# Kernel optimization log

Measured on AMD Instinct MI355X. Metric: run time of the kernel, lower is better.

Reference implementation:

```python
import jax, jax.numpy as jnp
import numpy as np

N, E, G, H, V, L = 100000, 1000000, 1000, 128, 64, 4
NEG_SLOPE = 0.2

def lrelu(x):
    return jnp.where(x >= 0, x, NEG_SLOPE * x)

def setup_inputs() -> dict:
    key = jax.random.key(0)
    ks = jax.random.split(key, 24)
    s = 0.05
    inp = {
        'nfeats': jax.random.randint(ks[0], (N, 9), 0, V, dtype=jnp.int32),
        'efeats': jax.random.randint(ks[1], (E, 3), 0, 4, dtype=jnp.int32),
        'src': jax.random.randint(ks[2], (E,), 0, N, dtype=jnp.int32),
        'dst': jax.random.randint(ks[3], (E,), 0, N, dtype=jnp.int32),
        'graph_ids': jnp.sort(jax.random.randint(ks[4], (N,), 0, G, dtype=jnp.int32)),
        'atom_emb': jax.random.normal(ks[5], (9, V, H), jnp.float32) * s,
        'Wq': jax.random.normal(ks[6], (L, H, H), jnp.float32) * s,
        'bq': jnp.zeros((L, H), jnp.float32),
        'Wk': jax.random.normal(ks[7], (L, H, H), jnp.float32) * s,
        'bk': jnp.zeros((L, H), jnp.float32),
        'Wr': jax.random.normal(ks[8], (L, H, H), jnp.float32) * s,
        'br': jnp.zeros((L, H), jnp.float32),
        'W1': jax.random.normal(ks[9], (H, H // 2), jnp.float32) * s,
        'b1': jnp.zeros((H // 2,), jnp.float32),
        'g1': jnp.ones((H // 2,), jnp.float32),
        'beta1': jnp.zeros((H // 2,), jnp.float32),
        'W2': jax.random.normal(ks[10], (H // 2, H // 4), jnp.float32) * s,
        'b2': jnp.zeros((H // 4,), jnp.float32),
        'g2': jnp.ones((H // 4,), jnp.float32),
        'beta2': jnp.zeros((H // 4,), jnp.float32),
        'W3': jax.random.normal(ks[11], (H // 4, 1), jnp.float32) * s,
        'b3': jnp.zeros((1,), jnp.float32),
    }
    return inp

def batchnorm(x, g, b):
    mu = jnp.mean(x, axis=0)
    var = jnp.var(x, axis=0)
    return (x - mu) * jax.lax.rsqrt(var + 1e-5) * g + b

def reference(nfeats, efeats, src, dst, graph_ids, atom_emb, Wq, bq, Wk, bk, Wr, br,
              W1, b1, g1, beta1, W2, b2, g2, beta2, W3, b3):
    # AtomEncoder: sum of per-feature embeddings -> [N, H]
    h = jnp.sum(atom_emb[jnp.arange(9)[None, :], nfeats], axis=1)
    for l in range(L):
        q = h @ Wq[l] + bq[l]            # dst-side transform [N,H]
        k = h @ Wk[l] + bk[l]            # src-side transform [N,H]
        m = lrelu(q[dst] + k[src])       # per-edge message [E,H]
        agg = jax.ops.segment_sum(m, dst, num_segments=N)  # [N,H]
        h = lrelu(agg @ Wr[l] + br[l])   # norm='none' -> identity, then activation
    hg = jax.ops.segment_sum(h, graph_ids, num_segments=G)  # sum pooling [G,H]
    x = lrelu(batchnorm(hg @ W1 + b1, g1, beta1))
    x = lrelu(batchnorm(x @ W2 + b2, g2, beta2))
    return x @ W3 + b3
```

## Files before the change

kernel.cpp:

```cpp
#include <hip/hip_runtime.h>

#define NN 100000
#define NP 100096
#define NE 1000000
#define NG 1000
#define H 128
#define NLAYER 4
#define NEG 0.2f
#define SCAN_BLOCKS 98

using short8 = __attribute__((ext_vector_type(8))) short;
using fx4 = __attribute__((ext_vector_type(4))) float;

__device__ __forceinline__ float lrelu(float x) { return x >= 0.f ? x : NEG * x; }

__device__ __forceinline__ unsigned short f2bf(float f) {
    union { float f; unsigned int u; } v;
    v.f = f;
    return (unsigned short)((v.u + 0x7fffu + ((v.u >> 16) & 1u)) >> 16);
}
__device__ __forceinline__ float bf2f(unsigned short h) {
    union { unsigned int u; float f; } v;
    v.u = ((unsigned int)h) << 16;
    return v.f;
}
__device__ __forceinline__ float bflo(unsigned int u) {
    union { unsigned int x; float f; } v;
    v.x = u << 16;
    return v.f;
}
__device__ __forceinline__ float bfhi(unsigned int u) {
    union { unsigned int x; float f; } v;
    v.x = u & 0xffff0000u;
    return v.f;
}

__global__ __launch_bounds__(256) void k_atom(const int* __restrict__ nfeats,
                                              const float* __restrict__ emb,
                                              unsigned short* __restrict__ h) {
    int node = blockIdx.x * 4 + (threadIdx.x >> 6);
    if (node >= NN) return;
    int lane = threadIdx.x & 63;
    int c = lane * 2;
    float ax = 0.f, ay = 0.f;
#pragma unroll
    for (int f = 0; f < 9; ++f) {
        int idx = nfeats[node * 9 + f];
        float2 e = *(const float2*)(emb + (size_t)((f << 6) + idx) * H + c);
        ax += e.x;
        ay += e.y;
    }
    unsigned int packed = (unsigned int)f2bf(ax) | ((unsigned int)f2bf(ay) << 16);
    *(unsigned int*)(h + (size_t)node * H + c) = packed;
}

__global__ __launch_bounds__(256) void k_wt(const float* __restrict__ Wq,
                                            const float* __restrict__ Wk,
                                            const float* __restrict__ Wr,
                                            unsigned short* __restrict__ WT) {
    int mat = blockIdx.x;
    int l = mat / 3;
    int kind = mat - l * 3;
    const float* src = (kind == 0 ? Wq : kind == 1 ? Wk : Wr) + (size_t)l * H * H;
    unsigned short* dst = WT + (size_t)mat * H * H;
    for (int idx = threadIdx.x; idx < H * H; idx += 256) {
        int kk = idx >> 7, n = idx & 127;
        dst[n * H + kk] = f2bf(src[idx]);
    }
}

__global__ __launch_bounds__(256) void k_hist(const int* __restrict__ dst, int* __restrict__ deg) {
    int i = blockIdx.x * blockDim.x + threadIdx.x;
    if (i < NE) atomicAdd(&deg[dst[i]], 1);
}

__global__ __launch_bounds__(1024) void k_scan1(const int* __restrict__ deg,
                                                int* __restrict__ rowp,
                                                int* __restrict__ bsum) {
    __shared__ int tmp[1024];
    int t = threadIdx.x;
    int i = blockIdx.x * 1024 + t;
    int v = (i < NN) ? deg[i] : 0;
    tmp[t] = v;
    __syncthreads();
    for (int off = 1; off < 1024; off <<= 1) {
        int u = (t >= off) ? tmp[t - off] : 0;
        __syncthreads();
        tmp[t] += u;
        __syncthreads();
    }
    if (i < NN) rowp[i] = tmp[t] - v;
    if (t == 1023) bsum[blockIdx.x] = tmp[1023];
}

__global__ __launch_bounds__(128) void k_scan2(int* __restrict__ bsum) {
    __shared__ int tmp[128];
    int t = threadIdx.x;
    int v = (t < SCAN_BLOCKS) ? bsum[t] : 0;
    tmp[t] = v;
    __syncthreads();
    for (int off = 1; off < 128; off <<= 1) {
        int u = (t >= off) ? tmp[t - off] : 0;
        __syncthreads();
        tmp[t] += u;
        __syncthreads();
    }
    if (t < SCAN_BLOCKS) bsum[t] = tmp[t] - v;
}

__global__ __launch_bounds__(256) void k_scan3(const int* __restrict__ bsum,
                                               int* __restrict__ rowp,
                                               int* __restrict__ cursor) {
    int i = blockIdx.x * blockDim.x + threadIdx.x;
    if (i < NN) {
        int v = rowp[i] + bsum[i >> 10];
        rowp[i] = v;
        cursor[i] = v;
    }
    if (i == 0) rowp[NN] = NE;
}

__global__ __launch_bounds__(256) void k_scatter(const int* __restrict__ src,
                                                 const int* __restrict__ dst,
                                                 int* __restrict__ cursor,
                                                 int* __restrict__ csr_src) {
    int i = blockIdx.x * blockDim.x + threadIdx.x;
    if (i < NE) {
        int pos = atomicAdd(&cursor[dst[i]], 1);
        csr_src[pos] = src[i];
    }
}

__global__ __launch_bounds__(256) void k_gbound(const int* __restrict__ gid,
                                                int* __restrict__ gstart) {
    int g = blockIdx.x * blockDim.x + threadIdx.x;
    if (g > NG) return;
    if (g == NG) { gstart[NG] = NN; return; }
    int lo = 0, hi = NN;
    while (lo < hi) {
        int mid = (lo + hi) >> 1;
        if (gid[mid] < g) lo = mid + 1; else hi = mid;
    }
    gstart[g] = lo;
}

__global__ __launch_bounds__(256) void k_qk_mfma(const unsigned short* __restrict__ h,
                                                 const unsigned short* __restrict__ WTq,
                                                 const float* __restrict__ bq,
                                                 const unsigned short* __restrict__ WTk,
                                                 const float* __restrict__ bk,
                                                 unsigned short* __restrict__ q,
                                                 unsigned short* __restrict__ k) {
    int lane = threadIdx.x & 63;
    int wave = threadIdx.x >> 6;
    int row0 = blockIdx.x * 128 + wave * 32;
    int lrow = lane & 15;
    int lk = (lane >> 4) << 3;

    short8 a[2][4];
#pragma unroll
    for (int rt = 0; rt < 2; ++rt)
#pragma unroll
        for (int ks = 0; ks < 4; ++ks)
            a[rt][ks] = *(const short8*)(h + (size_t)(row0 + rt * 16 + lrow) * H + ks * 32 + lk);

    fx4 aq[2][8], ak[2][8];
#pragma unroll
    for (int ct = 0; ct < 8; ++ct) {
        float vq = bq[ct * 16 + lrow];
        float vk = bk[ct * 16 + lrow];
#pragma unroll
        for (int rt = 0; rt < 2; ++rt) {
            aq[rt][ct] = fx4{vq, vq, vq, vq};
            ak[rt][ct] = fx4{vk, vk, vk, vk};
        }
    }

#pragma unroll
    for (int ks = 0; ks < 4; ++ks)
#pragma unroll
        for (int ct = 0; ct < 8; ++ct) {
            short8 wq = *(const short8*)(WTq + (ct * 16 + lrow) * H + ks * 32 + lk);
            short8 wk = *(const short8*)(WTk + (ct * 16 + lrow) * H + ks * 32 + lk);
#pragma unroll
            for (int rt = 0; rt < 2; ++rt) {
                aq[rt][ct] = __builtin_amdgcn_mfma_f32_16x16x32_bf16(a[rt][ks], wq, aq[rt][ct], 0, 0, 0);
                ak[rt][ct] = __builtin_amdgcn_mfma_f32_16x16x32_bf16(a[rt][ks], wk, ak[rt][ct], 0, 0, 0);
            }
        }

#pragma unroll
    for (int rt = 0; rt < 2; ++rt)
#pragma unroll
        for (int ct = 0; ct < 8; ++ct)
#pragma unroll
            for (int rg = 0; rg < 4; ++rg) {
                int r = row0 + rt * 16 + ((lane >> 4) << 2) + rg;
                if (r < NN) {
                    q[(size_t)r * H + ct * 16 + lrow] = f2bf(aq[rt][ct][rg]);
                    k[(size_t)r * H + ct * 16 + lrow] = f2bf(ak[rt][ct][rg]);
                }
            }
}

__global__ __launch_bounds__(256) void k_r_mfma(const unsigned short* __restrict__ agg,
                                                const unsigned short* __restrict__ WTr,
                                                const float* __restrict__ br,
                                                unsigned short* __restrict__ hout) {
    int lane = threadIdx.x & 63;
    int wave = threadIdx.x >> 6;
    int row0 = blockIdx.x * 128 + wave * 32;
    int lrow = lane & 15;
    int lk = (lane >> 4) << 3;

    short8 a[2][4];
#pragma unroll
    for (int rt = 0; rt < 2; ++rt)
#pragma unroll
        for (int ks = 0; ks < 4; ++ks)
            a[rt][ks] = *(const short8*)(agg + (size_t)(row0 + rt * 16 + lrow) * H + ks * 32 + lk);

    fx4 acc[2][8];
#pragma unroll
    for (int ct = 0; ct < 8; ++ct) {
        float v = br[ct * 16 + lrow];
#pragma unroll
        for (int rt = 0; rt < 2; ++rt) acc[rt][ct] = fx4{v, v, v, v};
    }

#pragma unroll
    for (int ks = 0; ks < 4; ++ks)
#pragma unroll
        for (int ct = 0; ct < 8; ++ct) {
            short8 w = *(const short8*)(WTr + (ct * 16 + lrow) * H + ks * 32 + lk);
#pragma unroll
            for (int rt = 0; rt < 2; ++rt)
                acc[rt][ct] = __builtin_amdgcn_mfma_f32_16x16x32_bf16(a[rt][ks], w, acc[rt][ct], 0, 0, 0);
        }

#pragma unroll
    for (int rt = 0; rt < 2; ++rt)
#pragma unroll
        for (int ct = 0; ct < 8; ++ct)
#pragma unroll
            for (int rg = 0; rg < 4; ++rg) {
                int r = row0 + rt * 16 + ((lane >> 4) << 2) + rg;
                if (r < NN)
                    hout[(size_t)r * H + ct * 16 + lrow] = f2bf(lrelu(acc[rt][ct][rg]));
            }
}

__global__ __launch_bounds__(256) void k_rqk_mfma(const unsigned short* __restrict__ agg,
                                                  const unsigned short* __restrict__ WTr,
                                                  const float* __restrict__ br,
                                                  const unsigned short* __restrict__ WTq,
                                                  const float* __restrict__ bq,
                                                  const unsigned short* __restrict__ WTk,
                                                  const float* __restrict__ bk,
                                                  unsigned short* __restrict__ q,
                                                  unsigned short* __restrict__ k) {
    __shared__ unsigned short hls[4][32][136];
    int lane = threadIdx.x & 63;
    int wave = threadIdx.x >> 6;
    int row0 = blockIdx.x * 128 + wave * 32;
    int lrow = lane & 15;
    int lk = (lane >> 4) << 3;

    short8 a[2][4];
#pragma unroll
    for (int rt = 0; rt < 2; ++rt)
#pragma unroll
        for (int ks = 0; ks < 4; ++ks)
            a[rt][ks] = *(const short8*)(agg + (size_t)(row0 + rt * 16 + lrow) * H + ks * 32 + lk);

    fx4 acc[2][8];
#pragma unroll
    for (int ct = 0; ct < 8; ++ct) {
        float v = br[ct * 16 + lrow];
#pragma unroll
        for (int rt = 0; rt < 2; ++rt) acc[rt][ct] = fx4{v, v, v, v};
    }

#pragma unroll
    for (int ks = 0; ks < 4; ++ks)
#pragma unroll
        for (int ct = 0; ct < 8; ++ct) {
            short8 w = *(const short8*)(WTr + (ct * 16 + lrow) * H + ks * 32 + lk);
#pragma unroll
            for (int rt = 0; rt < 2; ++rt)
                acc[rt][ct] = __builtin_amdgcn_mfma_f32_16x16x32_bf16(a[rt][ks], w, acc[rt][ct], 0, 0, 0);
        }

#pragma unroll
    for (int rt = 0; rt < 2; ++rt)
#pragma unroll
        for (int ct = 0; ct < 8; ++ct)
#pragma unroll
            for (int rg = 0; rg < 4; ++rg) {
                int lr = rt * 16 + ((lane >> 4) << 2) + rg;
                hls[wave][lr][ct * 16 + lrow] = f2bf(lrelu(acc[rt][ct][rg]));
            }

    short8 a2[2][4];
#pragma unroll
    for (int rt = 0; rt < 2; ++rt)
#pragma unroll
        for (int ks = 0; ks < 4; ++ks)
            a2[rt][ks] = *(const short8*)&hls[wave][rt * 16 + lrow][ks * 32 + lk];

    fx4 aq[2][8], ak[2][8];
#pragma unroll
    for (int ct = 0; ct < 8; ++ct) {
        float vq = bq[ct * 16 + lrow];
        float vk = bk[ct * 16 + lrow];
#pragma unroll
        for (int rt = 0; rt < 2; ++rt) {
            aq[rt][ct] = fx4{vq, vq, vq, vq};
            ak[rt][ct] = fx4{vk, vk, vk, vk};
        }
    }

#pragma unroll
    for (int ks = 0; ks < 4; ++ks)
#pragma unroll
        for (int ct = 0; ct < 8; ++ct) {
            short8 wq = *(const short8*)(WTq + (ct * 16 + lrow) * H + ks * 32 + lk);
            short8 wk = *(const short8*)(WTk + (ct * 16 + lrow) * H + ks * 32 + lk);
#pragma unroll
            for (int rt = 0; rt < 2; ++rt) {
                aq[rt][ct] = __builtin_amdgcn_mfma_f32_16x16x32_bf16(a2[rt][ks], wq, aq[rt][ct], 0, 0, 0);
                ak[rt][ct] = __builtin_amdgcn_mfma_f32_16x16x32_bf16(a2[rt][ks], wk, ak[rt][ct], 0, 0, 0);
            }
        }

#pragma unroll
    for (int rt = 0; rt < 2; ++rt)
#pragma unroll
        for (int ct = 0; ct < 8; ++ct)
#pragma unroll
            for (int rg = 0; rg < 4; ++rg) {
                int r = row0 + rt * 16 + ((lane >> 4) << 2) + rg;
                if (r < NN) {
                    q[(size_t)r * H + ct * 16 + lrow] = f2bf(aq[rt][ct][rg]);
                    k[(size_t)r * H + ct * 16 + lrow] = f2bf(ak[rt][ct][rg]);
                }
            }
}

__global__ __launch_bounds__(256) void k_agg(const unsigned short* __restrict__ q,
                                             const unsigned short* __restrict__ kk,
                                             const int* __restrict__ rowp,
                                             const int* __restrict__ csr_src,
                                             unsigned short* __restrict__ agg) {
    int node = blockIdx.x * 4 + (threadIdx.x >> 6);
    if (node >= NN) return;
    int lane = threadIdx.x & 63;
    int qt = lane >> 4;
    int ql = lane & 15;
    int start = rowp[node];
    int end = rowp[node + 1];

    uint4 qp = *(const uint4*)(q + (size_t)node * H + ql * 8);
    float qv0 = bflo(qp.x), qv1 = bfhi(qp.x), qv2 = bflo(qp.y), qv3 = bfhi(qp.y);
    float qv4 = bflo(qp.z), qv5 = bfhi(qp.z), qv6 = bflo(qp.w), qv7 = bfhi(qp.w);
    float a0 = 0.f, a1 = 0.f, a2 = 0.f, a3 = 0.f, a4 = 0.f, a5 = 0.f, a6 = 0.f, a7 = 0.f;

    for (int base = start; base < end; base += 64) {
        int cnt = end - base;
        if (cnt > 64) cnt = 64;
        int sid = (lane < cnt) ? csr_src[base + lane] : 0;
        int cnt4 = (cnt + 3) & ~3;
        for (int j = 0; j < cnt4; j += 4) {
            int jj = j + qt;
            int s = __shfl(sid, jj);
            uint4 kp = *(const uint4*)(kk + (size_t)s * H + ql * 8);
            if (jj < cnt) {
                a0 += lrelu(qv0 + bflo(kp.x));
                a1 += lrelu(qv1 + bfhi(kp.x));
                a2 += lrelu(qv2 + bflo(kp.y));
                a3 += lrelu(qv3 + bfhi(kp.y));
                a4 += lrelu(qv4 + bflo(kp.z));
                a5 += lrelu(qv5 + bfhi(kp.z));
                a6 += lrelu(qv6 + bflo(kp.w));
                a7 += lrelu(qv7 + bfhi(kp.w));
            }
        }
    }
    a0 += __shfl_xor(a0, 16); a0 += __shfl_xor(a0, 32);
    a1 += __shfl_xor(a1, 16); a1 += __shfl_xor(a1, 32);
    a2 += __shfl_xor(a2, 16); a2 += __shfl_xor(a2, 32);
    a3 += __shfl_xor(a3, 16); a3 += __shfl_xor(a3, 32);
    a4 += __shfl_xor(a4, 16); a4 += __shfl_xor(a4, 32);
    a5 += __shfl_xor(a5, 16); a5 += __shfl_xor(a5, 32);
    a6 += __shfl_xor(a6, 16); a6 += __shfl_xor(a6, 32);
    a7 += __shfl_xor(a7, 16); a7 += __shfl_xor(a7, 32);
    if (qt == 0) {
        uint4 o;
        o.x = (unsigned int)f2bf(a0) | ((unsigned int)f2bf(a1) << 16);
        o.y = (unsigned int)f2bf(a2) | ((unsigned int)f2bf(a3) << 16);
        o.z = (unsigned int)f2bf(a4) | ((unsigned int)f2bf(a5) << 16);
        o.w = (unsigned int)f2bf(a6) | ((unsigned int)f2bf(a7) << 16);
        *(uint4*)(agg + (size_t)node * H + ql * 8) = o;
    }
}

__global__ __launch_bounds__(256) void k_pool_seg(const unsigned short* __restrict__ h,
                                                  const int* __restrict__ gstart,
                                                  float* __restrict__ hg) {
    int g = blockIdx.x * 4 + (threadIdx.x >> 6);
    if (g >= NG) return;
    int lane = threadIdx.x & 63;
    int s = gstart[g], e = gstart[g + 1];
    float ax = 0.f, ay = 0.f;
    for (int n = s; n < e; ++n) {
        unsigned int hp = *(const unsigned int*)(h + (size_t)n * H + lane * 2);
        ax += bflo(hp);
        ay += bfhi(hp);
    }
    float2 o;
    o.x = ax;
    o.y = ay;
    *(float2*)(hg + (size_t)g * H + lane * 2) = o;
}

__global__ __launch_bounds__(256) void k_mlp1(const float* __restrict__ hg,
                                              const float* __restrict__ W1,
                                              const float* __restrict__ b1,
                                              float* __restrict__ x1) {
    __shared__ float W1s[128 * 64];
    __shared__ float hgs[4 * 128];
    int t = threadIdx.x;
    int g0 = blockIdx.x * 4;
#pragma unroll
    for (int i = 0; i < 32; ++i) W1s[t + i * 256] = W1[t + i * 256];
    for (int i = t; i < 4 * 128; i += 256) hgs[i] = hg[(size_t)g0 * H + i];
    __syncthreads();
    int g = t >> 6, c = t & 63;
    float acc = b1[c];
    const float* row = hgs + g * 128;
    for (int j = 0; j < 128; ++j) acc += row[j] * W1s[j * 64 + c];
    x1[(g0 + g) * 64 + c] = acc;
}

template <int C>
__global__ __launch_bounds__(1024) void k_bnstats(const float* __restrict__ x,
                                                  float* __restrict__ stats) {
    __shared__ float red[1024];
    __shared__ float mus[C];
    int t = threadIdx.x;
    int c = t & (C - 1), rc = t / C;
    const int R = 1024 / C;
    float s = 0.f;
    for (int g = rc; g < NG; g += R) s += x[g * C + c];
    red[t] = s;
    __syncthreads();
    if (t < C) {
        float S = 0.f;
        for (int i = 0; i < R; ++i) S += red[i * C + t];
        float mu = S / NG;
        mus[t] = mu;
        stats[t] = mu;
    }
    __syncthreads();
    float mu = mus[c];
    float s2 = 0.f;
    for (int g = rc; g < NG; g += R) {
        float d = x[g * C + c] - mu;
        s2 += d * d;
    }
    red[t] = s2;
    __syncthreads();
    if (t < C) {
        float Q = 0.f;
        for (int i = 0; i < R; ++i) Q += red[i * C + t];
        stats[C + t] = rsqrtf(Q / NG + 1e-5f);
    }
}

__global__ __launch_bounds__(256) void k_mlp2f(const float* __restrict__ x1,
                                               const float* __restrict__ st,
                                               const float* __restrict__ g1,
                                               const float* __restrict__ be1,
                                               const float* __restrict__ W2,
                                               const float* __restrict__ b2,
                                               float* __restrict__ x2) {
    __shared__ float W2s[64 * 32];
    __shared__ float x1s[8 * 64];
    int t = threadIdx.x;
    int g0 = blockIdx.x * 8;
#pragma unroll
    for (int i = 0; i < 8; ++i) W2s[t + i * 256] = W2[t + i * 256];
#pragma unroll
    for (int i = 0; i < 2; ++i) {
        int idx = t + i * 256;
        int c = idx & 63;
        float v = x1[(size_t)g0 * 64 + idx];
        v = (v - st[c]) * st[64 + c] * g1[c] + be1[c];
        x1s[idx] = lrelu(v);
    }
    __syncthreads();
    int g = t >> 5, c = t & 31;
    float acc = b2[c];
    const float* row = x1s + g * 64;
    for (int j = 0; j < 64; ++j) acc += row[j] * W2s[j * 32 + c];
    x2[(g0 + g) * 32 + c] = acc;
}

__global__ __launch_bounds__(256) void k_mlp3f(const float* __restrict__ x2,
                                               const float* __restrict__ st,
                                               const float* __restrict__ g2,
                                               const float* __restrict__ be2,
                                               const float* __restrict__ W3,
                                               const float* __restrict__ b3,
                                               float* __restrict__ out) {
    int g = blockIdx.x * blockDim.x + threadIdx.x;
    if (g >= NG) return;
    float acc = b3[0];
    for (int j = 0; j < 32; ++j) {
        float v = (x2[g * 32 + j] - st[j]) * st[32 + j] * g2[j] + be2[j];
        acc += lrelu(v) * W3[j];
    }
    out[g] = acc;
}

extern "C" void kernel_launch(void* const* d_in, const int* in_sizes, int n_in,
                              void* d_out, int out_size, void* d_ws, size_t ws_size,
                              hipStream_t stream) {
    const int* nfeats = (const int*)d_in[0];
    const int* src = (const int*)d_in[2];
    const int* dst = (const int*)d_in[3];
    const int* gid = (const int*)d_in[4];
    const float* emb = (const float*)d_in[5];
    const float* Wq = (const float*)d_in[6];
    const float* bq = (const float*)d_in[7];
    const float* Wk = (const float*)d_in[8];
    const float* bk = (const float*)d_in[9];
    const float* Wr = (const float*)d_in[10];
    const float* br = (const float*)d_in[11];
    const float* W1 = (const float*)d_in[12];
    const float* b1 = (const float*)d_in[13];
    const float* g1 = (const float*)d_in[14];
    const float* be1 = (const float*)d_in[15];
    const float* W2 = (const float*)d_in[16];
    const float* b2 = (const float*)d_in[17];
    const float* g2 = (const float*)d_in[18];
    const float* be2 = (const float*)d_in[19];
    const float* W3 = (const float*)d_in[20];
    const float* b3 = (const float*)d_in[21];
    float* out = (float*)d_out;

    size_t nh = (size_t)NP * H;
    unsigned short* P0 = (unsigned short*)d_ws;
    unsigned short* P1 = P0 + nh;
    unsigned short* P2 = P1 + nh;
    unsigned short* WT = P2 + nh;
    float* hg = (float*)(WT + 12 * H * H);
    float* x1 = hg + (size_t)NG * H;
    float* x2 = x1 + (size_t)NG * 64;
    float* st = x2 + (size_t)NG * 32;
    int* cursor = (int*)(st + 2 * 64);
    int* rowp = cursor + NN;
    int* bsum = rowp + NN + 1;
    int* csr_src = bsum + 128;
    int* gstart = csr_src + NE;

    hipMemsetAsync(cursor, 0, NN * sizeof(int), stream);
    k_hist<<<(NE + 255) / 256, 256, 0, stream>>>(dst, cursor);
    k_scan1<<<SCAN_BLOCKS, 1024, 0, stream>>>(cursor, rowp, bsum);
    k_scan2<<<1, 128, 0, stream>>>(bsum);
    k_scan3<<<(NN + 255) / 256, 256, 0, stream>>>(bsum, rowp, cursor);
    k_scatter<<<(NE + 255) / 256, 256, 0, stream>>>(src, dst, cursor, csr_src);
    k_gbound<<<(NG + 256) / 256, 256, 0, stream>>>(gid, gstart);

    k_wt<<<12, 256, 0, stream>>>(Wq, Wk, Wr, WT);
    k_atom<<<NN / 4, 256, 0, stream>>>(nfeats, emb, P0);

    const int NB = NP / 128;
    k_qk_mfma<<<NB, 256, 0, stream>>>(P0, WT + 0 * H * H, bq, WT + 1 * H * H, bk, P1, P2);
    for (int l = 0; l < NLAYER; ++l) {
        k_agg<<<(NN + 3) / 4, 256, 0, stream>>>(P1, P2, rowp, csr_src, P0);
        if (l < NLAYER - 1) {
            k_rqk_mfma<<<NB, 256, 0, stream>>>(P0, WT + (size_t)(l * 3 + 2) * H * H, br + l * H,
                                               WT + (size_t)((l + 1) * 3 + 0) * H * H, bq + (l + 1) * H,
                                               WT + (size_t)((l + 1) * 3 + 1) * H * H, bk + (l + 1) * H,
                                               P1, P2);
        } else {
            k_r_mfma<<<NB, 256, 0, stream>>>(P0, WT + (size_t)(l * 3 + 2) * H * H, br + l * H, P1);
        }
    }

    k_pool_seg<<<(NG + 3) / 4, 256, 0, stream>>>(P1, gstart, hg);

    k_mlp1<<<NG / 4, 256, 0, stream>>>(hg, W1, b1, x1);
    k_bnstats<64><<<1, 1024, 0, stream>>>(x1, st);
    k_mlp2f<<<NG / 8, 256, 0, stream>>>(x1, st, g1, be1, W2, b2, x2);
    k_bnstats<32><<<1, 1024, 0, stream>>>(x2, st);
    k_mlp3f<<<(NG + 255) / 256, 256, 0, stream>>>(x2, st, g2, be2, W3, b3, out);
}
```

Baseline: 752.8 us.

## Vectorize CSR build kernels, fuse graph-bound search, unroll aggregation gathers by two

The histogram and scatter kernels now each handle four edges per thread using int4 loads. The graph-boundary binary search is folded into the scan3 kernel as extra blocks, removing one launch. In the aggregation kernel, the edge loop is unrolled so each lane issues two independent K-row gathers per iteration, giving more memory-level parallelism. Together these aim to reduce launch count and memory latency stalls, at the cost of slightly more register pressure and padded iterations in aggregation.

```diff
diff --git a/kernel.cpp b/kernel.cpp
--- a/kernel.cpp
+++ b/kernel.cpp
@@ -71,7 +71,12 @@
 
 __global__ __launch_bounds__(256) void k_hist(const int* __restrict__ dst, int* __restrict__ deg) {
     int i = blockIdx.x * blockDim.x + threadIdx.x;
-    if (i < NE) atomicAdd(&deg[dst[i]], 1);
+    if (i * 4 >= NE) return;
+    int4 d = *(const int4*)(dst + i * 4);
+    atomicAdd(&deg[d.x], 1);
+    atomicAdd(&deg[d.y], 1);
+    atomicAdd(&deg[d.z], 1);
+    atomicAdd(&deg[d.w], 1);
 }
 
 __global__ __launch_bounds__(1024) void k_scan1(const int* __restrict__ deg,
@@ -108,16 +113,33 @@
     if (t < SCAN_BLOCKS) bsum[t] = tmp[t] - v;
 }
 
-__global__ __launch_bounds__(256) void k_scan3(const int* __restrict__ bsum,
-                                               int* __restrict__ rowp,
-                                               int* __restrict__ cursor) {
-    int i = blockIdx.x * blockDim.x + threadIdx.x;
-    if (i < NN) {
-        int v = rowp[i] + bsum[i >> 10];
-        rowp[i] = v;
-        cursor[i] = v;
-    }
-    if (i == 0) rowp[NN] = NE;
+#define SCAN3_BLOCKS ((NN + 255) / 256)
+__global__ __launch_bounds__(256) void k_scan3g(const int* __restrict__ bsum,
+                                                int* __restrict__ rowp,
+                                                int* __restrict__ cursor,
+                                                const int* __restrict__ gid,
+                                                int* __restrict__ gstart) {
+    int bid = blockIdx.x;
+    int t = threadIdx.x;
+    if (bid < SCAN3_BLOCKS) {
+        int i = bid * 256 + t;
+        if (i < NN) {
+            int v = rowp[i] + bsum[i >> 10];
+            rowp[i] = v;
+            cursor[i] = v;
+        }
+        if (i == 0) rowp[NN] = NE;
+    } else {
+        int g = (bid - SCAN3_BLOCKS) * 256 + t;
+        if (g > NG) return;
+        if (g == NG) { gstart[NG] = NN; return; }
+        int lo = 0, hi = NN;
+        while (lo < hi) {
+            int mid = (lo + hi) >> 1;
+            if (gid[mid] < g) lo = mid + 1; else hi = mid;
+        }
+        gstart[g] = lo;
+    }
 }
 
 __global__ __launch_bounds__(256) void k_scatter(const int* __restrict__ src,
@@ -125,23 +147,13 @@
                                                  int* __restrict__ cursor,
                                                  int* __restrict__ csr_src) {
     int i = blockIdx.x * blockDim.x + threadIdx.x;
-    if (i < NE) {
-        int pos = atomicAdd(&cursor[dst[i]], 1);
-        csr_src[pos] = src[i];
-    }
-}
-
-__global__ __launch_bounds__(256) void k_gbound(const int* __restrict__ gid,
-                                                int* __restrict__ gstart) {
-    int g = blockIdx.x * blockDim.x + threadIdx.x;
-    if (g > NG) return;
-    if (g == NG) { gstart[NG] = NN; return; }
-    int lo = 0, hi = NN;
-    while (lo < hi) {
-        int mid = (lo + hi) >> 1;
-        if (gid[mid] < g) lo = mid + 1; else hi = mid;
-    }
-    gstart[g] = lo;
+    if (i * 4 >= NE) return;
+    int4 s = *(const int4*)(src + i * 4);
+    int4 d = *(const int4*)(dst + i * 4);
+    csr_src[atomicAdd(&cursor[d.x], 1)] = s.x;
+    csr_src[atomicAdd(&cursor[d.y], 1)] = s.y;
+    csr_src[atomicAdd(&cursor[d.z], 1)] = s.z;
+    csr_src[atomicAdd(&cursor[d.w], 1)] = s.w;
 }
 
 __global__ __launch_bounds__(256) void k_qk_mfma(const unsigned short* __restrict__ h,
@@ -369,20 +381,33 @@
         int cnt = end - base;
         if (cnt > 64) cnt = 64;
         int sid = (lane < cnt) ? csr_src[base + lane] : 0;
-        int cnt4 = (cnt + 3) & ~3;
-        for (int j = 0; j < cnt4; j += 4) {
-            int jj = j + qt;
-            int s = __shfl(sid, jj);
-            uint4 kp = *(const uint4*)(kk + (size_t)s * H + ql * 8);
-            if (jj < cnt) {
-                a0 += lrelu(qv0 + bflo(kp.x));
-                a1 += lrelu(qv1 + bfhi(kp.x));
-                a2 += lrelu(qv2 + bflo(kp.y));
-                a3 += lrelu(qv3 + bfhi(kp.y));
-                a4 += lrelu(qv4 + bflo(kp.z));
-                a5 += lrelu(qv5 + bfhi(kp.z));
-                a6 += lrelu(qv6 + bflo(kp.w));
-                a7 += lrelu(qv7 + bfhi(kp.w));
+        int cnt8 = (cnt + 7) & ~7;
+        for (int j = 0; j < cnt8; j += 8) {
+            int jj0 = j + qt;
+            int jj1 = j + 4 + qt;
+            int s0 = __shfl(sid, jj0);
+            int s1 = __shfl(sid, jj1);
+            uint4 kp0 = *(const uint4*)(kk + (size_t)s0 * H + ql * 8);
+            uint4 kp1 = *(const uint4*)(kk + (size_t)s1 * H + ql * 8);
+            if (jj0 < cnt) {
+                a0 += lrelu(qv0 + bflo(kp0.x));
+                a1 += lrelu(qv1 + bfhi(kp0.x));
+                a2 += lrelu(qv2 + bflo(kp0.y));
+                a3 += lrelu(qv3 + bfhi(kp0.y));
+                a4 += lrelu(qv4 + bflo(kp0.z));
+                a5 += lrelu(qv5 + bfhi(kp0.z));
+                a6 += lrelu(qv6 + bflo(kp0.w));
+                a7 += lrelu(qv7 + bfhi(kp0.w));
+            }
+            if (jj1 < cnt) {
+                a0 += lrelu(qv0 + bflo(kp1.x));
+                a1 += lrelu(qv1 + bfhi(kp1.x));
+                a2 += lrelu(qv2 + bflo(kp1.y));
+                a3 += lrelu(qv3 + bfhi(kp1.y));
+                a4 += lrelu(qv4 + bflo(kp1.z));
+                a5 += lrelu(qv5 + bfhi(kp1.z));
+                a6 += lrelu(qv6 + bflo(kp1.w));
+                a7 += lrelu(qv7 + bfhi(kp1.w));
             }
         }
     }
@@ -565,12 +590,11 @@
     int* gstart = csr_src + NE;
 
     hipMemsetAsync(cursor, 0, NN * sizeof(int), stream);
-    k_hist<<<(NE + 255) / 256, 256, 0, stream>>>(dst, cursor);
+    k_hist<<<(NE / 4 + 255) / 256, 256, 0, stream>>>(dst, cursor);
     k_scan1<<<SCAN_BLOCKS, 1024, 0, stream>>>(cursor, rowp, bsum);
     k_scan2<<<1, 128, 0, stream>>>(bsum);
-    k_scan3<<<(NN + 255) / 256, 256, 0, stream>>>(bsum, rowp, cursor);
-    k_scatter<<<(NE + 255) / 256, 256, 0, stream>>>(src, dst, cursor, csr_src);
-    k_gbound<<<(NG + 256) / 256, 256, 0, stream>>>(gid, gstart);
+    k_scan3g<<<SCAN3_BLOCKS + 4, 256, 0, stream>>>(bsum, rowp, cursor, gid, gstart);
+    k_scatter<<<(NE / 4 + 255) / 256, 256, 0, stream>>>(src, dst, cursor, csr_src);
 
     k_wt<<<12, 256, 0, stream>>>(Wq, Wk, Wr, WT);
     k_atom<<<NN / 4, 256, 0, stream>>>(nfeats, emb, P0);
```

Result: faster. 734.7 us (-2.4%).
